# Kernel tuning notes

Measured on AMD Instinct MI355X. Metric: run time of the kernel, lower is better.

Reference implementation:

```python
import jax, jax.numpy as jnp
import numpy as np

N_ATOMS = 8000
N_PAIRS = 80000
NF_IN = 32
NF_OUT = 32
N_DIST = 16
N_COMP = 4      # l_max=1: [l=0 (1), l=1 (3)] tensor components
N_INV = 2       # _invariant_counts[(2, 1)]
MIND_SOFT = 0.85
MAXD_SOFT = 5.0
HARD_CUTOFF = 6.5
GN_EPS = 1e-5


def _sensitivity(dist, mu, sigma):
    # HIP-NN style inverse-distance Gaussians with smooth cos^2 cutoff.
    inv_d = 1.0 / dist                                   # (P,)
    base = jnp.exp(-0.5 * ((inv_d[:, None] - mu) / sigma) ** 2)  # (P, n_dist)
    cut = jnp.where(dist < HARD_CUTOFF,
                    jnp.cos(0.5 * jnp.pi * dist / HARD_CUTOFF) ** 2, 0.0)
    return base * cut[:, None]


def setup_inputs() -> dict:
    key = jax.random.key(0)
    ks = jax.random.split(key, 10)
    in_features = jax.random.normal(ks[0], (N_ATOMS, NF_IN), jnp.float32)
    pair_first = jnp.sort(jax.random.randint(ks[1], (N_PAIRS,), 0, N_ATOMS))
    pair_second = jax.random.randint(ks[2], (N_PAIRS,), 0, N_ATOMS)
    dist_pairs = (0.5 + (HARD_CUTOFF - 0.5)
                  * jax.random.uniform(ks[3], (N_PAIRS,), jnp.float32))
    tensor_rhats = jax.random.normal(ks[4], (N_PAIRS, N_COMP), jnp.float32)
    # learned params
    sens_mu = jnp.linspace(1.0 / MAXD_SOFT, 1.0 / MIND_SOFT, N_DIST).astype(jnp.float32)
    sens_sigma = jnp.full((N_DIST,), float(sens_mu[1] - sens_mu[0]), jnp.float32)
    s_int = (2.0 / (N_DIST * NF_IN + NF_OUT)) ** 0.5
    int_weights = s_int * jax.random.normal(ks[5], (N_DIST, NF_OUT, NF_IN), jnp.float32)
    s_self = (2.0 / (NF_IN + NF_OUT)) ** 0.5
    selfint_w = s_self * jax.random.normal(ks[6], (NF_OUT, NF_IN), jnp.float32)
    selfint_b = jnp.zeros((NF_OUT,), jnp.float32)
    s_mix = (2.0 / (N_INV * NF_OUT + NF_OUT)) ** 0.5
    mixing_weights = s_mix * jax.random.normal(ks[7], (NF_OUT, N_INV, NF_OUT), jnp.float32)
    gn_weight = jnp.ones((N_INV * NF_OUT,), jnp.float32)
    gn_bias = jnp.zeros((N_INV * NF_OUT,), jnp.float32)
    return {
        "in_features": in_features, "tensor_rhats": tensor_rhats,
        "dist_pairs": dist_pairs, "int_weights": int_weights,
        "selfint_w": selfint_w, "selfint_b": selfint_b,
        "mixing_weights": mixing_weights, "gn_weight": gn_weight,
        "gn_bias": gn_bias, "sens_mu": sens_mu, "sens_sigma": sens_sigma,
        "pair_first": pair_first, "pair_second": pair_second,
    }


def reference(in_features, tensor_rhats, dist_pairs, int_weights,
              selfint_w, selfint_b, mixing_weights, gn_weight, gn_bias,
              sens_mu, sens_sigma, pair_first, pair_second):
    n_atoms = in_features.shape[0]
    # self interaction (Linear)
    self_part = in_features @ selfint_w.T + selfint_b          # (N, nf_out)
    # tensor sensitivities: (P, n_comp, n_dist) -> flat (P, n_comp*n_dist)
    sense = _sensitivity(dist_pairs, sens_mu, sens_sigma)      # (P, n_dist)
    sense_flat = (tensor_rhats[:, :, None] * sense[:, None, :]).reshape(
        -1, N_COMP * N_DIST)
    # envsum: env[a, s, f] = sum_{p: pair_first[p]=a} sense_flat[p, s] * feat[pair_second[p], f]
    feat_j = in_features[pair_second]                          # (P, nf_in)
    contrib = sense_flat[:, :, None] * feat_j[:, None, :]      # (P, S, nf_in)
    env = jax.ops.segment_sum(contrib, pair_first, num_segments=n_atoms)
    # interaction weights contraction
    w_rs = jnp.transpose(int_weights, (0, 2, 1)).reshape(N_DIST * NF_IN, NF_OUT)
    env_rs = env.reshape(n_atoms * N_COMP, N_DIST * NF_IN)
    tf = (env_rs @ w_rs).reshape(n_atoms, N_COMP, NF_OUT)
    tf = jnp.transpose(tf, (0, 2, 1))                          # (N, nf_out, n_comp)
    # HopInvariantLayer (n_max=2, l_max=1): [l=0 scalar, |l=1 vector|^2]
    invariants = jnp.stack(
        [tf[..., 0], jnp.sum(tf[..., 1:] ** 2, axis=-1)], axis=-1)  # (N, nf_out, 2)
    # GroupNorm over channels (n_inv groups of nf_out channels)
    x = jnp.transpose(invariants, (0, 2, 1))                   # (N, n_inv, nf_out)
    mean = jnp.mean(x, axis=-1, keepdims=True)
    var = jnp.var(x, axis=-1, keepdims=True)
    xn = (x - mean) / jnp.sqrt(var + GN_EPS)
    xn = xn * gn_weight.reshape(N_INV, NF_OUT) + gn_bias.reshape(N_INV, NF_OUT)
    norm_inv = jnp.transpose(xn, (0, 2, 1)).reshape(n_atoms, NF_OUT * N_INV)
    mix = norm_inv @ mixing_weights.reshape(NF_OUT * N_INV, NF_OUT)
    return mix + self_part
```

## Files before the change

kernel.cpp:

```cpp
#include <hip/hip_runtime.h>
#include <hip/hip_bf16.h>
#include <stdint.h>

#define GN_EPS 1e-5f

typedef __fp16 half2_t __attribute__((ext_vector_type(2)));
typedef __fp16 v8h __attribute__((ext_vector_type(8)));
typedef float v4f __attribute__((ext_vector_type(4)));
union U32H2 { uint32_t u; half2_t h; };
union U4V8 { uint4 u; v8h h; };

__device__ __forceinline__ float ldin(const void* p, int i, bool bf) {
    if (bf) {
        uint32_t u = (uint32_t)((const uint16_t*)p)[i];
        union { uint32_t u; float f; } c; c.u = u << 16;
        return c.f;
    }
    return ((const float*)p)[i];
}

__device__ __forceinline__ uint16_t f2bf(float x) {
    union { float f; uint32_t u; } c; c.f = x;
    uint32_t u = c.u;
    return (uint16_t)((u + 0x7FFFu + ((u >> 16) & 1u)) >> 16);
}

__device__ __forceinline__ bool detect_bf16(const void* gnw) {
    uint32_t det = *(const uint32_t*)gnw;
    return (det >> 16) == (det & 0xFFFFu);
}

__device__ __forceinline__ uint32_t pkh2(float lo, float hi) {
    U32H2 u; u.h = __builtin_amdgcn_cvt_pkrtz(lo, hi); return u.u;
}

__global__ __launch_bounds__(256) void k0_prep(
    const void* __restrict__ feat, const void* __restrict__ rhats,
    const void* __restrict__ dists, const void* __restrict__ intw,
    const void* __restrict__ selfw, const void* __restrict__ selfb,
    const void* __restrict__ mw, const void* __restrict__ gnw,
    const void* __restrict__ gnb, const void* __restrict__ mu,
    const void* __restrict__ sig, const int* __restrict__ pf,
    int* __restrict__ seg, uint32_t* __restrict__ Wmf,
    float* __restrict__ featf, float4* __restrict__ rc4,
    float2* __restrict__ dj2, const int* __restrict__ ps,
    float* __restrict__ mwf, float* __restrict__ selfwf,
    float* __restrict__ gnwf, float* __restrict__ gnbf,
    float* __restrict__ selfbf, float* __restrict__ muf,
    float* __restrict__ isgf, int n_atoms, int n_pairs)
{
    const bool bf = detect_bf16(gnw);
    const int tid = blockIdx.x * 256 + threadIdx.x;

    if (tid < n_pairs) {
        int a0 = pf[tid];
        if (tid == 0) { for (int a = 0; a <= a0; ++a) seg[a] = 0; }
        if (tid + 1 < n_pairs) {
            int a1 = pf[tid + 1];
            for (int a = a0 + 1; a <= a1; ++a) seg[a] = tid + 1;
        } else {
            for (int a = a0 + 1; a <= n_atoms; ++a) seg[a] = n_pairs;
        }
        float dist = ldin(dists, tid, bf);
        float cd = __cosf(0.2416609733530613f * dist);
        float cut = (dist < 6.5f) ? cd * cd : 0.0f;
        float4 rc;
        rc.x = ldin(rhats, 4 * tid + 0, bf) * cut;
        rc.y = ldin(rhats, 4 * tid + 1, bf) * cut;
        rc.z = ldin(rhats, 4 * tid + 2, bf) * cut;
        rc.w = ldin(rhats, 4 * tid + 3, bf) * cut;
        rc4[tid] = rc;
        float2 dj; dj.x = 1.0f / dist; dj.y = __int_as_float(ps[tid]);
        dj2[tid] = dj;
    }
    {
        int i0 = tid * 4;
#pragma unroll
        for (int k = 0; k < 4; ++k) {
            int i = i0 + k;
            if (i < n_atoms * 32) featf[i] = ldin(feat, i, bf);
        }
    }
    if (tid < 8192) {
        int fp = tid & 15, d = (tid >> 4) & 15, o = tid >> 8;
        float wlo = ldin(intw, (d * 32 + o) * 32 + 2 * fp, bf);
        float whi = ldin(intw, (d * 32 + o) * 32 + 2 * fp + 1, bf);
        Wmf[tid] = pkh2(wlo, whi);
    }
    if (tid < 2048) mwf[tid] = ldin(mw, tid, bf);
    if (tid < 1024) selfwf[tid] = ldin(selfw, tid, bf);
    if (tid < 64) { gnwf[tid] = ldin(gnw, tid, bf); gnbf[tid] = ldin(gnb, tid, bf); }
    if (tid < 32) selfbf[tid] = ldin(selfb, tid, bf);
    if (tid < 16) { muf[tid] = ldin(mu, tid, bf); isgf[tid] = 1.0f / ldin(sig, tid, bf); }
}

__global__ __launch_bounds__(256, 4) void k2_main(
    const int* __restrict__ seg, const uint32_t* __restrict__ Wmf,
    const float* __restrict__ featf, const float4* __restrict__ rc4,
    const float2* __restrict__ dj2, const float* __restrict__ mwf,
    const float* __restrict__ selfwf, const float* __restrict__ gnwf,
    const float* __restrict__ gnbf, const float* __restrict__ selfbf,
    const float* __restrict__ muf, const float* __restrict__ isgf,
    const void* __restrict__ gnw, void* __restrict__ out, int n_atoms)
{
    __shared__ uint32_t envs[16 * 256];
    __shared__ float tfs[4 * 32 * 4];
    __shared__ float mwTs[32 * 68];
    __shared__ float xns[4][64];

    const int t = threadIdx.x, wv = t >> 6, lane = t & 63;
    int a = blockIdx.x * 4 + wv;
    const bool astore = (a < n_atoms);
    if (!astore) a = n_atoms - 1;

    {
        int o = t & 31, kc = t >> 5;
#pragma unroll
        for (int i = 0; i < 8; ++i) {
            int k = kc * 8 + i;
            mwTs[o * 68 + k] = mwf[k * 32 + o];
        }
    }

    const int dD = lane >> 2, fq = lane & 3;
    const float mu_d = muf[dD], isg_d = isgf[dD];

    float env[4][8];
#pragma unroll
    for (int c = 0; c < 4; ++c)
#pragma unroll
        for (int fl = 0; fl < 8; ++fl) env[c][fl] = 0.0f;

    const int s = seg[a], e = seg[a + 1];

    for (int p = s; p < e; p += 4) {
        float2 dj[4]; float4 rc[4];
#pragma unroll
        for (int i = 0; i < 4; ++i) {
            int pi = (p + i < e) ? p + i : e - 1;
            dj[i] = dj2[pi];
            float4 r = rc4[pi];
            if (p + i >= e) r = make_float4(0.f, 0.f, 0.f, 0.f);
            rc[i] = r;
        }
        float4 fa[4], fb[4];
#pragma unroll
        for (int i = 0; i < 4; ++i) {
            const float4* fr = (const float4*)(featf +
                (size_t)__float_as_int(dj[i].y) * 32) + fq * 2;
            fa[i] = fr[0]; fb[i] = fr[1];
        }
#pragma unroll
        for (int i = 0; i < 4; ++i) {
            float x = (dj[i].x - mu_d) * isg_d;
            float sd = __expf(-0.5f * x * x);
            float t0 = sd * rc[i].x, t1 = sd * rc[i].y;
            float t2 = sd * rc[i].z, t3 = sd * rc[i].w;
            float fj[8] = {fa[i].x, fa[i].y, fa[i].z, fa[i].w,
                           fb[i].x, fb[i].y, fb[i].z, fb[i].w};
#pragma unroll
            for (int fl = 0; fl < 8; ++fl) {
                env[0][fl] = fmaf(t0, fj[fl], env[0][fl]);
                env[1][fl] = fmaf(t1, fj[fl], env[1][fl]);
                env[2][fl] = fmaf(t2, fj[fl], env[2][fl]);
                env[3][fl] = fmaf(t3, fj[fl], env[3][fl]);
            }
        }
    }

    {
        const int ci = dD * 4 + fq;
#pragma unroll
        for (int c = 0; c < 4; ++c) {
            int m = wv * 4 + c;
            uint4 w;
            w.x = pkh2(env[c][0], env[c][1]);
            w.y = pkh2(env[c][2], env[c][3]);
            w.z = pkh2(env[c][4], env[c][5]);
            w.w = pkh2(env[c][6], env[c][7]);
            *(uint4*)&envs[m * 256 + ((ci ^ m) << 2)] = w;
        }
    }
    __syncthreads();

    if ((wv & 1) == 0) {
        const int tile = wv >> 1;
        const int mrow = lane & 15, quad = lane >> 4;
        v4f acc = {0.f, 0.f, 0.f, 0.f};
        const uint4* wb = (const uint4*)Wmf + ((tile * 16 + mrow) * 64 + quad);
#pragma unroll
        for (int kk = 0; kk < 16; ++kk) {
            int cia = kk * 4 + quad;
            U4V8 Af, Bf;
            Af.u = *(const uint4*)&envs[mrow * 256 + ((cia ^ mrow) << 2)];
            Bf.u = wb[kk * 4];
            acc = __builtin_amdgcn_mfma_f32_16x16x32_f16(Af.h, Bf.h, acc, 0, 0, 0);
        }
        float4 st; st.x = acc[0]; st.y = acc[1]; st.z = acc[2]; st.w = acc[3];
        *(float4*)&tfs[(quad * 32 + tile * 16 + mrow) * 4] = st;
    }
    __syncthreads();

    const int o = lane & 31, half = lane >> 5;
    float4 tf = *(const float4*)&tfs[(wv * 32 + o) * 4];
    float inv0 = tf.x;
    float inv1 = tf.y * tf.y + tf.z * tf.z + tf.w * tf.w;

    float s0 = inv0, q0 = inv0 * inv0, s1 = inv1, q1 = inv1 * inv1;
#pragma unroll
    for (int m = 16; m >= 1; m >>= 1) {
        s0 += __shfl_xor(s0, m, 32);
        q0 += __shfl_xor(q0, m, 32);
        s1 += __shfl_xor(s1, m, 32);
        q1 += __shfl_xor(q1, m, 32);
    }
    float mean0 = s0 * (1.f / 32.f), mean1 = s1 * (1.f / 32.f);
    float var0 = q0 * (1.f / 32.f) - mean0 * mean0;
    float var1 = q1 * (1.f / 32.f) - mean1 * mean1;
    float xn0 = (inv0 - mean0) * rsqrtf(var0 + GN_EPS);
    float xn1 = (inv1 - mean1) * rsqrtf(var1 + GN_EPS);
    xn0 = xn0 * gnwf[o] + gnbf[o];
    xn1 = xn1 * gnwf[32 + o] + gnbf[32 + o];

    if (half == 0) {
        *(float2*)&xns[wv][2 * o] = make_float2(xn0, xn1);
    }

    float mix = 0.0f;
#pragma unroll
    for (int c = 0; c < 16; ++c) {
        float4 xk = *(const float4*)&xns[wv][c * 4];
        float4 w4 = *(const float4*)&mwTs[o * 68 + c * 4];
        mix = fmaf(xk.x, w4.x, mix);
        mix = fmaf(xk.y, w4.y, mix);
        mix = fmaf(xk.z, w4.z, mix);
        mix = fmaf(xk.w, w4.w, mix);
    }

    float sacc = selfbf[o];
    const float4* fr4 = (const float4*)(featf + (size_t)a * 32);
    const float4* sw4 = (const float4*)(selfwf + o * 32);
#pragma unroll
    for (int k = 0; k < 8; ++k) {
        float4 fv = fr4[k], w4 = sw4[k];
        sacc = fmaf(fv.x, w4.x, sacc);
        sacc = fmaf(fv.y, w4.y, sacc);
        sacc = fmaf(fv.z, w4.z, sacc);
        sacc = fmaf(fv.w, w4.w, sacc);
    }

    float res = mix + sacc;
    if (half == 0 && astore) {
        if (detect_bf16(gnw)) ((uint16_t*)out)[a * 32 + o] = f2bf(res);
        else                  ((float*)out)[a * 32 + o]    = res;
    }
}

extern "C" void kernel_launch(void* const* d_in, const int* in_sizes, int n_in,
                              void* d_out, int out_size, void* d_ws, size_t ws_size,
                              hipStream_t stream) {
    const void* feat  = d_in[0];
    const void* rhats = d_in[1];
    const void* dists = d_in[2];
    const void* intw  = d_in[3];
    const void* selfw = d_in[4];
    const void* selfb = d_in[5];
    const void* mw    = d_in[6];
    const void* gnw   = d_in[7];
    const void* gnb   = d_in[8];
    const void* mu    = d_in[9];
    const void* sig   = d_in[10];
    const int* pf     = (const int*)d_in[11];
    const int* ps     = (const int*)d_in[12];

    const int n_pairs = in_sizes[11];
    const int n_atoms = in_sizes[0] / 32;

    char* ws = (char*)d_ws;
    int*      seg    = (int*)(ws + 0);
    uint32_t* Wmf    = (uint32_t*)(ws + 32768);
    float*    featf  = (float*)(ws + 65536);
    float4*   rc4    = (float4*)(ws + 1089536);
    float2*   dj2    = (float2*)(ws + 2369536);
    float*    mwf    = (float*)(ws + 3009536);
    float*    selfwf = (float*)(ws + 3017728);
    float*    gnwf   = (float*)(ws + 3021824);
    float*    gnbf   = (float*)(ws + 3022080);
    float*    selfbf = (float*)(ws + 3022336);
    float*    muf    = (float*)(ws + 3022464);
    float*    isgf   = (float*)(ws + 3022528);

    int thr = n_pairs;
    int feat_thr = (n_atoms * 32 + 3) / 4;
    if (feat_thr > thr) thr = feat_thr;
    if (thr < 8192) thr = 8192;
    hipLaunchKernelGGL(k0_prep, dim3((thr + 255) / 256), dim3(256), 0, stream,
                       feat, rhats, dists, intw, selfw, selfb, mw, gnw, gnb,
                       mu, sig, pf, seg, Wmf, featf, rc4, dj2, ps, mwf,
                       selfwf, gnwf, gnbf, selfbf, muf, isgf, n_atoms, n_pairs);
    hipLaunchKernelGGL(k2_main, dim3((n_atoms + 3) / 4), dim3(256), 0, stream,
                       seg, Wmf, featf, rc4, dj2, mwf, selfwf, gnwf, gnbf,
                       selfbf, muf, isgf, gnw, d_out, n_atoms);
}
```

Baseline: 113.4 us.

## Fuse per-pair preprocessing into main kernel and use MFMA for self-interaction

Drops the per-pair and feature precomputation from the prep kernel. The main kernel now reads raw dists, rhats, pair indices and features directly (bf16 or fp32 via a templated path) and computes the cutoff and inverse distance inline. This removes the workspace round trip of those intermediate arrays. The otherwise idle odd waves now compute the self-interaction with a single MFMA in fp16 instead of a scalar dot product. The transposed mixing weights are read from global memory rather than staged in LDS, and occupancy is raised to 5 blocks. The cost is recomputing cos/rcp per pair per wave lane group and lower precision in the self term.

```diff
diff --git a/kernel.cpp b/kernel.cpp
--- a/kernel.cpp
+++ b/kernel.cpp
@@ -9,11 +9,11 @@
 typedef float v4f __attribute__((ext_vector_type(4)));
 union U32H2 { uint32_t u; half2_t h; };
 union U4V8 { uint4 u; v8h h; };
+union UF { uint32_t u; float f; };
 
 __device__ __forceinline__ float ldin(const void* p, int i, bool bf) {
     if (bf) {
-        uint32_t u = (uint32_t)((const uint16_t*)p)[i];
-        union { uint32_t u; float f; } c; c.u = u << 16;
+        UF c; c.u = ((uint32_t)((const uint16_t*)p)[i]) << 16;
         return c.f;
     }
     return ((const float*)p)[i];
@@ -35,16 +35,13 @@
 }
 
 __global__ __launch_bounds__(256) void k0_prep(
-    const void* __restrict__ feat, const void* __restrict__ rhats,
-    const void* __restrict__ dists, const void* __restrict__ intw,
-    const void* __restrict__ selfw, const void* __restrict__ selfb,
-    const void* __restrict__ mw, const void* __restrict__ gnw,
-    const void* __restrict__ gnb, const void* __restrict__ mu,
-    const void* __restrict__ sig, const int* __restrict__ pf,
+    const void* __restrict__ intw, const void* __restrict__ selfw,
+    const void* __restrict__ selfb, const void* __restrict__ mw,
+    const void* __restrict__ gnw, const void* __restrict__ gnb,
+    const void* __restrict__ mu, const void* __restrict__ sig,
+    const int* __restrict__ pf,
     int* __restrict__ seg, uint32_t* __restrict__ Wmf,
-    float* __restrict__ featf, float4* __restrict__ rc4,
-    float2* __restrict__ dj2, const int* __restrict__ ps,
-    float* __restrict__ mwf, float* __restrict__ selfwf,
+    uint32_t* __restrict__ selfh, float* __restrict__ mwT,
     float* __restrict__ gnwf, float* __restrict__ gnbf,
     float* __restrict__ selfbf, float* __restrict__ muf,
     float* __restrict__ isgf, int n_atoms, int n_pairs)
@@ -61,25 +58,6 @@
         } else {
             for (int a = a0 + 1; a <= n_atoms; ++a) seg[a] = n_pairs;
         }
-        float dist = ldin(dists, tid, bf);
-        float cd = __cosf(0.2416609733530613f * dist);
-        float cut = (dist < 6.5f) ? cd * cd : 0.0f;
-        float4 rc;
-        rc.x = ldin(rhats, 4 * tid + 0, bf) * cut;
-        rc.y = ldin(rhats, 4 * tid + 1, bf) * cut;
-        rc.z = ldin(rhats, 4 * tid + 2, bf) * cut;
-        rc.w = ldin(rhats, 4 * tid + 3, bf) * cut;
-        rc4[tid] = rc;
-        float2 dj; dj.x = 1.0f / dist; dj.y = __int_as_float(ps[tid]);
-        dj2[tid] = dj;
-    }
-    {
-        int i0 = tid * 4;
-#pragma unroll
-        for (int k = 0; k < 4; ++k) {
-            int i = i0 + k;
-            if (i < n_atoms * 32) featf[i] = ldin(feat, i, bf);
-        }
     }
     if (tid < 8192) {
         int fp = tid & 15, d = (tid >> 4) & 15, o = tid >> 8;
@@ -87,41 +65,112 @@
         float whi = ldin(intw, (d * 32 + o) * 32 + 2 * fp + 1, bf);
         Wmf[tid] = pkh2(wlo, whi);
     }
-    if (tid < 2048) mwf[tid] = ldin(mw, tid, bf);
-    if (tid < 1024) selfwf[tid] = ldin(selfw, tid, bf);
+    if (tid < 512) {
+        int fp = tid & 15, o = tid >> 4;
+        selfh[tid] = pkh2(ldin(selfw, o * 32 + 2 * fp, bf),
+                          ldin(selfw, o * 32 + 2 * fp + 1, bf));
+    }
+    if (tid < 2048) {
+        int k = tid & 63, o = tid >> 6;
+        mwT[tid] = ldin(mw, k * 32 + o, bf);
+    }
     if (tid < 64) { gnwf[tid] = ldin(gnw, tid, bf); gnbf[tid] = ldin(gnb, tid, bf); }
     if (tid < 32) selfbf[tid] = ldin(selfb, tid, bf);
     if (tid < 16) { muf[tid] = ldin(mu, tid, bf); isgf[tid] = 1.0f / ldin(sig, tid, bf); }
 }
 
-__global__ __launch_bounds__(256, 4) void k2_main(
+template <bool BF>
+__device__ __forceinline__ void ldfeat8(const void* feat, int j, int fq, float fj[8]) {
+    if (BF) {
+        uint4 q = *(const uint4*)((const uint16_t*)feat + (size_t)j * 32 + fq * 8);
+        uint32_t qd[4] = {q.x, q.y, q.z, q.w};
+#pragma unroll
+        for (int k = 0; k < 4; ++k) {
+            UF lo, hi; lo.u = qd[k] << 16; hi.u = qd[k] & 0xFFFF0000u;
+            fj[2 * k] = lo.f; fj[2 * k + 1] = hi.f;
+        }
+    } else {
+        const float4* fr = (const float4*)((const float*)feat + (size_t)j * 32) + fq * 2;
+        float4 a = fr[0], b = fr[1];
+        fj[0] = a.x; fj[1] = a.y; fj[2] = a.z; fj[3] = a.w;
+        fj[4] = b.x; fj[5] = b.y; fj[6] = b.z; fj[7] = b.w;
+    }
+}
+
+template <bool BF>
+__device__ __forceinline__ void pair_phase(
+    const void* __restrict__ feat, const void* __restrict__ rhats,
+    const void* __restrict__ dists, const int* __restrict__ ps,
+    int s, int e, int fq, float mu_d, float isg_d, float (&env)[4][8])
+{
+    for (int p = s; p < e; p += 4) {
+        int jj[4]; float4 rc[4]; float invd[4];
+#pragma unroll
+        for (int i = 0; i < 4; ++i) {
+            int pi = (p + i < e) ? p + i : e - 1;
+            jj[i] = ps[pi];
+            float dist, r0, r1, r2, r3;
+            if (BF) {
+                UF d16; d16.u = ((uint32_t)((const uint16_t*)dists)[pi]) << 16;
+                dist = d16.f;
+                uint2 rv = *(const uint2*)((const uint16_t*)rhats + 4 * pi);
+                UF e0, e1, e2, e3;
+                e0.u = rv.x << 16; e1.u = rv.x & 0xFFFF0000u;
+                e2.u = rv.y << 16; e3.u = rv.y & 0xFFFF0000u;
+                r0 = e0.f; r1 = e1.f; r2 = e2.f; r3 = e3.f;
+            } else {
+                dist = ((const float*)dists)[pi];
+                float4 rv = ((const float4*)rhats)[pi];
+                r0 = rv.x; r1 = rv.y; r2 = rv.z; r3 = rv.w;
+            }
+            float cd = __cosf(0.2416609733530613f * dist);
+            float cut = (dist < 6.5f) ? cd * cd : 0.0f;
+            if (p + i >= e) cut = 0.0f;
+            rc[i] = make_float4(r0 * cut, r1 * cut, r2 * cut, r3 * cut);
+            invd[i] = __builtin_amdgcn_rcpf(dist);
+        }
+        float fj[4][8];
+#pragma unroll
+        for (int i = 0; i < 4; ++i) ldfeat8<BF>(feat, jj[i], fq, fj[i]);
+#pragma unroll
+        for (int i = 0; i < 4; ++i) {
+            float x = (invd[i] - mu_d) * isg_d;
+            float sd = __expf(-0.5f * x * x);
+            float t0 = sd * rc[i].x, t1 = sd * rc[i].y;
+            float t2 = sd * rc[i].z, t3 = sd * rc[i].w;
+#pragma unroll
+            for (int fl = 0; fl < 8; ++fl) {
+                env[0][fl] = fmaf(t0, fj[i][fl], env[0][fl]);
+                env[1][fl] = fmaf(t1, fj[i][fl], env[1][fl]);
+                env[2][fl] = fmaf(t2, fj[i][fl], env[2][fl]);
+                env[3][fl] = fmaf(t3, fj[i][fl], env[3][fl]);
+            }
+        }
+    }
+}
+
+__global__ __launch_bounds__(256, 5) void k2_main(
     const int* __restrict__ seg, const uint32_t* __restrict__ Wmf,
-    const float* __restrict__ featf, const float4* __restrict__ rc4,
-    const float2* __restrict__ dj2, const float* __restrict__ mwf,
-    const float* __restrict__ selfwf, const float* __restrict__ gnwf,
-    const float* __restrict__ gnbf, const float* __restrict__ selfbf,
-    const float* __restrict__ muf, const float* __restrict__ isgf,
-    const void* __restrict__ gnw, void* __restrict__ out, int n_atoms)
+    const uint32_t* __restrict__ selfh, const float* __restrict__ mwT,
+    const void* __restrict__ feat, const void* __restrict__ rhats,
+    const void* __restrict__ dists, const int* __restrict__ ps,
+    const float* __restrict__ gnwf, const float* __restrict__ gnbf,
+    const float* __restrict__ selfbf, const float* __restrict__ muf,
+    const float* __restrict__ isgf, const void* __restrict__ gnw,
+    void* __restrict__ out, int n_atoms)
 {
     __shared__ uint32_t envs[16 * 256];
     __shared__ float tfs[4 * 32 * 4];
-    __shared__ float mwTs[32 * 68];
+    __shared__ float selfs[4][32];
     __shared__ float xns[4][64];
 
+    const bool bf = detect_bf16(gnw);
     const int t = threadIdx.x, wv = t >> 6, lane = t & 63;
-    int a = blockIdx.x * 4 + wv;
+    const int a0 = blockIdx.x * 4;
+    int a = a0 + wv;
     const bool astore = (a < n_atoms);
     if (!astore) a = n_atoms - 1;
 
-    {
-        int o = t & 31, kc = t >> 5;
-#pragma unroll
-        for (int i = 0; i < 8; ++i) {
-            int k = kc * 8 + i;
-            mwTs[o * 68 + k] = mwf[k * 32 + o];
-        }
-    }
-
     const int dD = lane >> 2, fq = lane & 3;
     const float mu_d = muf[dD], isg_d = isgf[dD];
 
@@ -132,41 +181,8 @@
         for (int fl = 0; fl < 8; ++fl) env[c][fl] = 0.0f;
 
     const int s = seg[a], e = seg[a + 1];
-
-    for (int p = s; p < e; p += 4) {
-        float2 dj[4]; float4 rc[4];
-#pragma unroll
-        for (int i = 0; i < 4; ++i) {
-            int pi = (p + i < e) ? p + i : e - 1;
-            dj[i] = dj2[pi];
-            float4 r = rc4[pi];
-            if (p + i >= e) r = make_float4(0.f, 0.f, 0.f, 0.f);
-            rc[i] = r;
-        }
-        float4 fa[4], fb[4];
-#pragma unroll
-        for (int i = 0; i < 4; ++i) {
-            const float4* fr = (const float4*)(featf +
-                (size_t)__float_as_int(dj[i].y) * 32) + fq * 2;
-            fa[i] = fr[0]; fb[i] = fr[1];
-        }
-#pragma unroll
-        for (int i = 0; i < 4; ++i) {
-            float x = (dj[i].x - mu_d) * isg_d;
-            float sd = __expf(-0.5f * x * x);
-            float t0 = sd * rc[i].x, t1 = sd * rc[i].y;
-            float t2 = sd * rc[i].z, t3 = sd * rc[i].w;
-            float fj[8] = {fa[i].x, fa[i].y, fa[i].z, fa[i].w,
-                           fb[i].x, fb[i].y, fb[i].z, fb[i].w};
-#pragma unroll
-            for (int fl = 0; fl < 8; ++fl) {
-                env[0][fl] = fmaf(t0, fj[fl], env[0][fl]);
-                env[1][fl] = fmaf(t1, fj[fl], env[1][fl]);
-                env[2][fl] = fmaf(t2, fj[fl], env[2][fl]);
-                env[3][fl] = fmaf(t3, fj[fl], env[3][fl]);
-            }
-        }
-    }
+    if (bf) pair_phase<true >(feat, rhats, dists, ps, s, e, fq, mu_d, isg_d, env);
+    else    pair_phase<false>(feat, rhats, dists, ps, s, e, fq, mu_d, isg_d, env);
 
     {
         const int ci = dD * 4 + fq;
@@ -183,9 +199,9 @@
     }
     __syncthreads();
 
+    const int mrow = lane & 15, quad = lane >> 4;
+    const int tile = wv >> 1;
     if ((wv & 1) == 0) {
-        const int tile = wv >> 1;
-        const int mrow = lane & 15, quad = lane >> 4;
         v4f acc = {0.f, 0.f, 0.f, 0.f};
         const uint4* wb = (const uint4*)Wmf + ((tile * 16 + mrow) * 64 + quad);
 #pragma unroll
@@ -198,6 +214,34 @@
         }
         float4 st; st.x = acc[0]; st.y = acc[1]; st.z = acc[2]; st.w = acc[3];
         *(float4*)&tfs[(quad * 32 + tile * 16 + mrow) * 4] = st;
+    } else {
+        int ar = a0 + (mrow < 4 ? mrow : 0);
+        if (ar >= n_atoms) ar = n_atoms - 1;
+        U4V8 Af, Bf;
+        if (bf) {
+            uint4 q = *(const uint4*)((const uint16_t*)feat + (size_t)ar * 32 + quad * 8);
+            uint32_t qd[4] = {q.x, q.y, q.z, q.w};
+            uint32_t r[4];
+#pragma unroll
+            for (int k = 0; k < 4; ++k) {
+                UF lo, hi; lo.u = qd[k] << 16; hi.u = qd[k] & 0xFFFF0000u;
+                r[k] = pkh2(lo.f, hi.f);
+            }
+            Af.u = make_uint4(r[0], r[1], r[2], r[3]);
+        } else {
+            const float4* fp4 = (const float4*)((const float*)feat + (size_t)ar * 32 + quad * 8);
+            float4 x = fp4[0], y = fp4[1];
+            Af.u = make_uint4(pkh2(x.x, x.y), pkh2(x.z, x.w),
+                              pkh2(y.x, y.y), pkh2(y.z, y.w));
+        }
+        Bf.u = *(const uint4*)(selfh + (tile * 16 + mrow) * 16 + quad * 4);
+        v4f acc = {0.f, 0.f, 0.f, 0.f};
+        acc = __builtin_amdgcn_mfma_f32_16x16x32_f16(Af.h, Bf.h, acc, 0, 0, 0);
+        if (quad == 0) {
+#pragma unroll
+            for (int r = 0; r < 4; ++r)
+                selfs[r][tile * 16 + mrow] = acc[r];
+        }
     }
     __syncthreads();
 
@@ -222,37 +266,24 @@
     xn0 = xn0 * gnwf[o] + gnbf[o];
     xn1 = xn1 * gnwf[32 + o] + gnbf[32 + o];
 
-    if (half == 0) {
-        *(float2*)&xns[wv][2 * o] = make_float2(xn0, xn1);
-    }
+    if (half == 0) *(float2*)&xns[wv][2 * o] = make_float2(xn0, xn1);
 
     float mix = 0.0f;
+    const float4* mrow4 = (const float4*)(mwT + o * 64);
 #pragma unroll
     for (int c = 0; c < 16; ++c) {
         float4 xk = *(const float4*)&xns[wv][c * 4];
-        float4 w4 = *(const float4*)&mwTs[o * 68 + c * 4];
+        float4 w4 = mrow4[c];
         mix = fmaf(xk.x, w4.x, mix);
         mix = fmaf(xk.y, w4.y, mix);
         mix = fmaf(xk.z, w4.z, mix);
         mix = fmaf(xk.w, w4.w, mix);
     }
 
-    float sacc = selfbf[o];
-    const float4* fr4 = (const float4*)(featf + (size_t)a * 32);
-    const float4* sw4 = (const float4*)(selfwf + o * 32);
-#pragma unroll
-    for (int k = 0; k < 8; ++k) {
-        float4 fv = fr4[k], w4 = sw4[k];
-        sacc = fmaf(fv.x, w4.x, sacc);
-        sacc = fmaf(fv.y, w4.y, sacc);
-        sacc = fmaf(fv.z, w4.z, sacc);
-        sacc = fmaf(fv.w, w4.w, sacc);
-    }
-
-    float res = mix + sacc;
+    float res = mix + selfs[wv][o] + selfbf[o];
     if (half == 0 && astore) {
-        if (detect_bf16(gnw)) ((uint16_t*)out)[a * 32 + o] = f2bf(res);
-        else                  ((float*)out)[a * 32 + o]    = res;
+        if (bf) ((uint16_t*)out)[a * 32 + o] = f2bf(res);
+        else    ((float*)out)[a * 32 + o]    = res;
     }
 }
 
@@ -279,26 +310,20 @@
     char* ws = (char*)d_ws;
     int*      seg    = (int*)(ws + 0);
     uint32_t* Wmf    = (uint32_t*)(ws + 32768);
-    float*    featf  = (float*)(ws + 65536);
-    float4*   rc4    = (float4*)(ws + 1089536);
-    float2*   dj2    = (float2*)(ws + 2369536);
-    float*    mwf    = (float*)(ws + 3009536);
-    float*    selfwf = (float*)(ws + 3017728);
-    float*    gnwf   = (float*)(ws + 3021824);
-    float*    gnbf   = (float*)(ws + 3022080);
-    float*    selfbf = (float*)(ws + 3022336);
-    float*    muf    = (float*)(ws + 3022464);
-    float*    isgf   = (float*)(ws + 3022528);
-
-    int thr = n_pairs;
-    int feat_thr = (n_atoms * 32 + 3) / 4;
-    if (feat_thr > thr) thr = feat_thr;
-    if (thr < 8192) thr = 8192;
+    uint32_t* selfh  = (uint32_t*)(ws + 65536);
+    float*    mwT    = (float*)(ws + 69632);
+    float*    gnwf   = (float*)(ws + 77824);
+    float*    gnbf   = (float*)(ws + 78080);
+    float*    selfbf = (float*)(ws + 78336);
+    float*    muf    = (float*)(ws + 78464);
+    float*    isgf   = (float*)(ws + 78528);
+
+    int thr = n_pairs < 8192 ? 8192 : n_pairs;
     hipLaunchKernelGGL(k0_prep, dim3((thr + 255) / 256), dim3(256), 0, stream,
-                       feat, rhats, dists, intw, selfw, selfb, mw, gnw, gnb,
-                       mu, sig, pf, seg, Wmf, featf, rc4, dj2, ps, mwf,
-                       selfwf, gnwf, gnbf, selfbf, muf, isgf, n_atoms, n_pairs);
+                       intw, selfw, selfb, mw, gnw, gnb, mu, sig, pf,
+                       seg, Wmf, selfh, mwT, gnwf, gnbf, selfbf, muf, isgf,
+                       n_atoms, n_pairs);
     hipLaunchKernelGGL(k2_main, dim3((n_atoms + 3) / 4), dim3(256), 0, stream,
-                       seg, Wmf, featf, rc4, dj2, mwf, selfwf, gnwf, gnbf,
-                       selfbf, muf, isgf, gnw, d_out, n_atoms);
-}
+                       seg, Wmf, selfh, mwT, feat, rhats, dists, ps,
+                       gnwf, gnbf, selfbf, muf, isgf, gnw, d_out, n_atoms);
+}
```

After: 116.8 us. 3.0% more time.
